# Kernel tuning notes

Measured on AMD Instinct MI355X. Metric: run time of the kernel, lower is better.

Reference implementation:

```python
import jax, jax.numpy as jnp
import numpy as np

N_NODES = 50000
N_EDGES = 640000
D_IN = 128
D_H1 = 128
D_H2 = 256
NEG_SLOPE = 0.2


def setup_inputs() -> dict:
    key = jax.random.key(0)
    ks = jax.random.split(key, 12)
    s = 1.0 / np.sqrt(D_IN)
    inp = {
        'x': jax.random.normal(ks[0], (N_NODES, D_IN), dtype=jnp.float32),
        'edge_index': jax.random.randint(ks[1], (2, N_EDGES), 0, N_NODES, dtype=jnp.int64),
        # GATv2 layer 1: 128 -> 128 (separate lin_l / lin_r, attention vec, residual proj, bias)
        'Wl1': jax.random.normal(ks[2], (D_IN, D_H1), dtype=jnp.float32) * s,
        'Wr1': jax.random.normal(ks[3], (D_IN, D_H1), dtype=jnp.float32) * s,
        'att1': jax.random.normal(ks[4], (D_H1,), dtype=jnp.float32) * s,
        'Wres1': jax.random.normal(ks[5], (D_IN, D_H1), dtype=jnp.float32) * s,
        'b1': jnp.zeros((D_H1,), dtype=jnp.float32),
        # GATv2 layer 2: 128 -> 256
        'Wl2': jax.random.normal(ks[6], (D_H1, D_H2), dtype=jnp.float32) * s,
        'Wr2': jax.random.normal(ks[7], (D_H1, D_H2), dtype=jnp.float32) * s,
        'att2': jax.random.normal(ks[8], (D_H2,), dtype=jnp.float32) * s,
        'Wres2': jax.random.normal(ks[9], (D_H1, D_H2), dtype=jnp.float32) * s,
        'b2': jnp.zeros((D_H2,), dtype=jnp.float32),
    }
    return inp


def _gatv2_layer(x, Wl, Wr, att, Wres, b, src, dst, n_nodes):
    """GATv2Conv (heads=1, residual=True, eval mode/no dropout).
    score e_ij = att . LeakyReLU(Wl x_src + Wr x_dst); softmax over incoming edges per dst;
    out_dst = sum_j alpha_ij * (Wl x_src) + residual + bias.
    """
    xl = x @ Wl                      # [N, F]
    xr = x @ Wr                      # [N, F]
    h = xl[src] + xr[dst]            # [E, F]  gather (irregular access)
    e = jax.nn.leaky_relu(h, NEG_SLOPE) @ att   # [E]
    # segment softmax over destination nodes
    m = jax.ops.segment_max(e, dst, num_segments=n_nodes)      # [N]
    w = jnp.exp(e - m[dst])                                     # [E]
    denom = jax.ops.segment_sum(w, dst, num_segments=n_nodes)   # [N]
    alpha = w / (denom[dst] + 1e-16)                             # [E]
    out = jax.ops.segment_sum(alpha[:, None] * xl[src], dst, num_segments=n_nodes)  # [N, F]
    return out + x @ Wres + b


def reference(x, edge_index, Wl1, Wr1, att1, Wres1, b1, Wl2, Wr2, att2, Wres2, b2):
    src = edge_index[0]
    dst = edge_index[1]
    h = _gatv2_layer(x, Wl1, Wr1, att1, Wres1, b1, src, dst, N_NODES)
    h = jax.nn.elu(h)
    out = _gatv2_layer(h, Wl2, Wr2, att2, Wres2, b2, src, dst, N_NODES)
    return out
```

## Files before the change

kernel.cpp:

```cpp
#include <hip/hip_runtime.h>

typedef unsigned short u16;
typedef unsigned int u32;
typedef __attribute__((ext_vector_type(8))) short bf16x8;
typedef __attribute__((ext_vector_type(4))) float f32x4;
typedef __attribute__((ext_vector_type(2))) float f32x2;

#define NN 50000
#define NE 640000

__device__ __forceinline__ float bfl(u32 u) { return __uint_as_float(u << 16); }
__device__ __forceinline__ float bfh(u32 u) { return __uint_as_float(u & 0xffff0000u); }
__device__ __forceinline__ float bf1(u16 v) { return __uint_as_float(((u32)v) << 16); }
__device__ __forceinline__ u16 f2bf(float f) {
  u32 u = __float_as_uint(f);
  u32 r = (u + 0x7fffu + ((u >> 16) & 1u)) >> 16;
  return (u16)r;
}

__device__ __forceinline__ f32x2 bc2(float s) { return (f32x2){s, s}; }
__device__ __forceinline__ f32x2 pkfma(f32x2 a, f32x2 b, f32x2 c) {
  return __builtin_elementwise_fma(a, b, c);
}
__device__ __forceinline__ f32x2 pkabs(f32x2 a) {
  return __builtin_elementwise_abs(a);
}

template <int CTRL>
__device__ __forceinline__ float dpp_add(float x) {
  int t = __builtin_amdgcn_update_dpp(0, __float_as_int(x), CTRL, 0xf, 0xf, true);
  return x + __int_as_float(t);
}

__device__ __forceinline__ void unpk2(uint4 v, f32x2* o) {
  o[0] = (f32x2){bfl(v.x), bfh(v.x)};
  o[1] = (f32x2){bfl(v.y), bfh(v.y)};
  o[2] = (f32x2){bfl(v.z), bfh(v.z)};
  o[3] = (f32x2){bfl(v.w), bfh(v.w)};
}

__global__ void probe_zero_kernel(const u16* __restrict__ x, const int* __restrict__ ei,
                                  int* __restrict__ flags, int* __restrict__ cnt, int n) {
  int g = blockIdx.x * 256 + threadIdx.x;
  if (g < n) cnt[g] = 0;
  if (blockIdx.x == 0) {
    __shared__ int s_f32, s_i32;
    if (threadIdx.x == 0) { s_f32 = 0; s_i32 = 0; }
    __syncthreads();
    int lf = 0, li = 0;
    for (int i = threadIdx.x; i < 1024; i += 256) {
      float v = bf1(x[i]);
      if (!(fabsf(v) < 1e8f)) lf = 1;
      if (ei[2 * i + 1] != 0) li = 1;
    }
    if (lf) s_f32 = 1;
    if (li) s_i32 = 1;
    __syncthreads();
    if (threadIdx.x == 0) {
      flags[0] = s_f32;
      flags[1] = s_i32 ? 0 : 1;
    }
  }
}

__device__ __forceinline__ int edge_val(const int* __restrict__ w, long j, int i64) {
  return i64 ? w[2 * j] : w[j];
}

__global__ void count_kernel(const int* __restrict__ ei, const int* __restrict__ flags,
                             int* __restrict__ cnt, int E) {
  int e = blockIdx.x * blockDim.x + threadIdx.x;
  if (e >= E) return;
  int d = edge_val(ei, (long)E + e, flags[1]);
  if ((u32)d < (u32)NN) atomicAdd(&cnt[d], 1);
}

__global__ void scan_local(const int* __restrict__ cnt, int* __restrict__ excl,
                           int* __restrict__ bsum, int n) {
  __shared__ int sd[256];
  int t = threadIdx.x;
  int g = blockIdx.x * 256 + t;
  int v = (g < n) ? cnt[g] : 0;
  sd[t] = v;
  __syncthreads();
  for (int off = 1; off < 256; off <<= 1) {
    int x = (t >= off) ? sd[t - off] : 0;
    __syncthreads();
    sd[t] += x;
    __syncthreads();
  }
  int incl = sd[t];
  if (g < n) excl[g] = incl - v;
  if (t == 255) bsum[blockIdx.x] = incl;
}

__global__ void scan_add(const int* __restrict__ excl, const int* __restrict__ bsum,
                         const int* __restrict__ cnt, int* __restrict__ rowptr,
                         int* __restrict__ fillp, int n, int nb) {
  __shared__ int sd[256];
  int t = threadIdx.x;
  sd[t] = (t < nb && t < (int)blockIdx.x) ? bsum[t] : 0;
  __syncthreads();
  for (int off = 128; off > 0; off >>= 1) {
    if (t < off) sd[t] += sd[t + off];
    __syncthreads();
  }
  int boff = sd[0];
  int g = blockIdx.x * 256 + t;
  if (g < n) {
    int e2 = excl[g] + boff;
    rowptr[g] = e2;
    fillp[g] = e2;
    if (g == n - 1) rowptr[n] = e2 + cnt[g];
  }
}

__global__ void fill_kernel(const int* __restrict__ ei, const int* __restrict__ flags,
                            int* __restrict__ fillp, int* __restrict__ col, int E) {
  int e = blockIdx.x * blockDim.x + threadIdx.x;
  if (e >= E) return;
  int i64 = flags[1];
  int s = edge_val(ei, (long)e, i64);
  int d = edge_val(ei, (long)E + e, i64);
  if ((u32)d >= (u32)NN) return;
  int p = atomicAdd(&fillp[d], 1);
  col[p] = ((u32)s < (u32)NN) ? s : 0;
}

__global__ void transpose_w(const void* W0, const void* W1, const void* W2,
                            const void* W3, const void* W4, const void* W5,
                            u16* T0, u16* T1, u16* T2, u16* T3, u16* T4, u16* T5,
                            const int* __restrict__ flags) {
  int y = blockIdx.y;
  int M = (y < 3) ? 128 : 256;
  int flat = blockIdx.x * 256 + threadIdx.x;
  if (flat >= M * 128) return;
  int j = flat >> 7;
  int k = flat & 127;
  const void* W = (y == 0) ? W0 : (y == 1) ? W1 : (y == 2) ? W2 : (y == 3) ? W3 : (y == 4) ? W4 : W5;
  u16* T = (y == 0) ? T0 : (y == 1) ? T1 : (y == 2) ? T2 : (y == 3) ? T3 : (y == 4) ? T4 : T5;
  u16 v;
  if (flags[0])
    v = f2bf(((const float*)W)[(size_t)k * M + j]);
  else
    v = ((const u16*)W)[(size_t)k * M + j];
  T[(size_t)j * 128 + k] = v;
}

#define LSTR 136
template <int MZ>
__global__ __launch_bounds__(256) void gemm3_mz(
    const void* __restrict__ X,
    const u16* __restrict__ Wta, const u16* __restrict__ Wtb, const u16* __restrict__ Wtc,
    const void* __restrict__ bias,
    u16* __restrict__ Ya, u16* __restrict__ Yb, u16* __restrict__ Yc,
    const int* __restrict__ flags, int x_follows, int N) {
  constexpr int M = MZ * 128;
  __shared__ __align__(16) u16 Xs[64 * LSTR];
  __shared__ __align__(16) u16 Bs[128 * LSTR];
  const int K = 128;
  int t = threadIdx.x;
  int lane = t & 63;
  int w = t >> 6;
  int n0g = blockIdx.x * 64;
  int F32X = x_follows ? flags[0] : 0;
  const u16* Wt = (blockIdx.y == 0) ? Wta : ((blockIdx.y == 1) ? Wtb : Wtc);
  u16* Y = (blockIdx.y == 0) ? Ya : ((blockIdx.y == 1) ? Yb : Yc);

  if (!F32X) {
    const u16* Xg = (const u16*)X;
    for (int it = 0; it < 4; ++it) {
      int i = t + 256 * it;
      int r = i >> 4, c8 = (i & 15) * 8;
      int n = n0g + r;
      uint4 v = make_uint4(0, 0, 0, 0);
      if (n < N) v = *(const uint4*)(Xg + (size_t)n * K + c8);
      *(uint4*)(Xs + r * LSTR + c8) = v;
    }
  } else {
    const float* Xg = (const float*)X;
    for (int it = 0; it < 4; ++it) {
      int i = t + 256 * it;
      int r = i >> 4, c8 = (i & 15) * 8;
      int n = n0g + r;
      uint4 pk = make_uint4(0, 0, 0, 0);
      if (n < N) {
        float4 f0 = *(const float4*)(Xg + (size_t)n * K + c8);
        float4 f1 = *(const float4*)(Xg + (size_t)n * K + c8 + 4);
        pk.x = (u32)f2bf(f0.x) | ((u32)f2bf(f0.y) << 16);
        pk.y = (u32)f2bf(f0.z) | ((u32)f2bf(f0.w) << 16);
        pk.z = (u32)f2bf(f1.x) | ((u32)f2bf(f1.y) << 16);
        pk.w = (u32)f2bf(f1.z) | ((u32)f2bf(f1.w) << 16);
      }
      *(uint4*)(Xs + r * LSTR + c8) = pk;
    }
  }

  int m0 = (w >> 1) * 32;
  int n0 = (w & 1) * 64;
  int l15 = lane & 15;
  int q8 = (lane >> 4) * 8;
  int F32B = flags[0];

#pragma unroll
  for (int z = 0; z < MZ; ++z) {
    int c0 = z * 128;
    for (int it = 0; it < 8; ++it) {
      int i = t + 256 * it;
      int j = i >> 4, k8 = (i & 15) * 8;
      uint4 v = *(const uint4*)(Wt + (size_t)(c0 + j) * K + k8);
      *(uint4*)(Bs + j * LSTR + k8) = v;
    }
    __syncthreads();

    f32x4 acc[2][4];
#pragma unroll
    for (int i = 0; i < 2; ++i)
#pragma unroll
      for (int j = 0; j < 4; ++j) acc[i][j] = (f32x4){0.f, 0.f, 0.f, 0.f};

#pragma unroll
    for (int kc = 0; kc < 4; ++kc) {
      int ko = kc * 32 + q8;
      bf16x8 a[2], b[4];
#pragma unroll
      for (int i = 0; i < 2; ++i)
        a[i] = *(const bf16x8*)(Xs + (m0 + i * 16 + l15) * LSTR + ko);
#pragma unroll
      for (int j = 0; j < 4; ++j)
        b[j] = *(const bf16x8*)(Bs + (n0 + j * 16 + l15) * LSTR + ko);
#pragma unroll
      for (int i = 0; i < 2; ++i)
#pragma unroll
        for (int j = 0; j < 4; ++j)
          acc[i][j] = __builtin_amdgcn_mfma_f32_16x16x32_bf16(a[i], b[j], acc[i][j], 0, 0, 0);
    }
    __syncthreads();

    float bv[4] = {0.f, 0.f, 0.f, 0.f};
    if (blockIdx.y == 2) {
#pragma unroll
      for (int j = 0; j < 4; ++j) {
        int c = c0 + n0 + j * 16 + l15;
        bv[j] = F32B ? ((const float*)bias)[c] : bf1(((const u16*)bias)[c]);
      }
    }

    u16* Ct = Bs;
#pragma unroll
    for (int i = 0; i < 2; ++i)
#pragma unroll
      for (int j = 0; j < 4; ++j) {
        int colj = n0 + j * 16 + l15;
        int rbase = m0 + i * 16 + (lane >> 4) * 4;
#pragma unroll
        for (int r = 0; r < 4; ++r)
          Ct[(rbase + r) * LSTR + colj] = f2bf(acc[i][j][r] + bv[j]);
      }
    __syncthreads();

    for (int it = 0; it < 4; ++it) {
      int i = t + 256 * it;
      int r = i >> 4, c8 = (i & 15) * 8;
      int n = n0g + r;
      if (n < N) {
        uint4 v = *(const uint4*)(Ct + r * LSTR + c8);
        *(uint4*)(Y + (size_t)n * M + c0 + c8) = v;
      }
    }
    __syncthreads();
  }
}

template <int F, bool ELU, int GL>
__global__ __launch_bounds__(256) void gat_agg_kernel(
    const u16* __restrict__ xl, const u16* __restrict__ xr, const u16* __restrict__ res,
    const void* __restrict__ att, const int* __restrict__ rowptr, const int* __restrict__ col,
    void* __restrict__ out, const int* __restrict__ flags, int out_follows, int N) {
  constexpr int HEPL = F / GL;
  constexpr int HP = HEPL / 2;
  static_assert(HEPL == 8, "GL must be F/8");
  int tid = threadIdx.x;
  int gl = tid & (GL - 1);
  int node = blockIdx.x * (256 / GL) + (tid / GL);
  if (node >= N) return;
  int F32 = flags[0];
  int OF32 = out_follows ? F32 : 0;
  int base = gl * HEPL;

  f32x2 xr2[HP], att6[HP], att4[HP], acc2[HP];
  {
    uint4 xp = *(const uint4*)(xr + (size_t)node * F + base);
    unpk2(xp, xr2);
  }
  if (F32) {
    const float* af = (const float*)att + base;
#pragma unroll
    for (int p = 0; p < HP; ++p) {
      f32x2 a = (f32x2){af[2 * p], af[2 * p + 1]};
      att6[p] = a * 0.6f;
      att4[p] = a * 0.4f;
    }
  } else {
    f32x2 a2[HP];
    uint4 ap = *(const uint4*)((const u16*)att + base);
    unpk2(ap, a2);
#pragma unroll
    for (int p = 0; p < HP; ++p) {
      att6[p] = a2[p] * 0.6f;
      att4[p] = a2[p] * 0.4f;
    }
  }
#pragma unroll
  for (int p = 0; p < HP; ++p) acc2[p] = bc2(0.f);

  float m = -1e30f, l = 0.f;
  int beg = rowptr[node], end = rowptr[node + 1];
  int deg = end - beg;

  if (deg > 0) {
    int nit = (deg + 1) >> 1;
    int dm1 = deg - 1;
    auto ldc = [&](int j) -> int { return col[beg + min(j, dm1)]; };
    auto gat = [&](int c) -> uint4 { return *(const uint4*)(xl + (size_t)c * F + base); };

    int c4 = ldc(4), c5 = ldc(5);
    uint4 va = gat(ldc(0)), vb = gat(ldc(1)), vc = gat(ldc(2)), vd = gat(ldc(3));

    for (int t = 0; t < nit; ++t) {
      uint4 x0v = va, x1v = vb;
      int act1 = (2 * t + 1) < deg;
      va = vc; vb = vd;
      if (t + 2 < nit) { vc = gat(c4); vd = gat(c5); }
      if (t + 3 < nit) { c4 = ldc(2 * t + 6); c5 = ldc(2 * t + 7); }

      f32x2 x0[HP], x1[HP];
      unpk2(x0v, x0);
      unpk2(x1v, x1);
      f32x2 s0 = bc2(0.f), s1 = bc2(0.f);
#pragma unroll
      for (int p = 0; p < HP; ++p) {
        f32x2 h0 = x0[p] + xr2[p];
        f32x2 h1 = x1[p] + xr2[p];
        f32x2 ha0 = pkabs(h0);
        f32x2 ha1 = pkabs(h1);
        s0 = pkfma(att6[p], h0, s0);
        s1 = pkfma(att6[p], h1, s1);
        s0 = pkfma(att4[p], ha0, s0);
        s1 = pkfma(att4[p], ha1, s1);
      }
      float d0 = s0.x + s0.y;
      float d1 = s1.x + s1.y;
      d0 = dpp_add<0xB1>(d0);  d1 = dpp_add<0xB1>(d1);
      d0 = dpp_add<0x4E>(d0);  d1 = dpp_add<0x4E>(d1);
      d0 = dpp_add<0x141>(d0); d1 = dpp_add<0x141>(d1);
      d0 = dpp_add<0x140>(d0); d1 = dpp_add<0x140>(d1);
      if constexpr (GL == 32) {
        d0 += __shfl_xor(d0, 16, 64);
        d1 += __shfl_xor(d1, 16, 64);
      }

      float p0 = d0;
      float p1 = act1 ? d1 : -1e30f;
      float mn = fmaxf(m, fmaxf(p0, p1));
      float scl = __expf(m - mn);
      float w0 = __expf(p0 - mn);
      float w1 = __expf(p1 - mn);
      l = fmaf(l, scl, w0 + w1);
      f32x2 w0b = bc2(w0), w1b = bc2(w1), sclb = bc2(scl);
#pragma unroll
      for (int p = 0; p < HP; ++p)
        acc2[p] = pkfma(sclb, acc2[p], pkfma(w1b, x1[p], w0b * x0[p]));
      m = mn;
    }
  }

  float inv = 1.f / (l + 1e-16f);
  uint4 rp = *(const uint4*)(res + (size_t)node * F + base);
  f32x2 rv[HP];
  unpk2(rp, rv);
  f32x2 ov[HP];
  f32x2 invb = bc2(inv);
#pragma unroll
  for (int p = 0; p < HP; ++p) {
    f32x2 o = pkfma(acc2[p], invb, rv[p]);
    if (ELU) {
      o.x = (o.x > 0.f) ? o.x : (__expf(o.x) - 1.f);
      o.y = (o.y > 0.f) ? o.y : (__expf(o.y) - 1.f);
    }
    ov[p] = o;
  }
  if (OF32) {
    float* of = (float*)out + (size_t)node * F + base;
    float4 f0 = {ov[0].x, ov[0].y, ov[1].x, ov[1].y};
    float4 f1 = {ov[2].x, ov[2].y, ov[3].x, ov[3].y};
    *(float4*)of = f0;
    *(float4*)(of + 4) = f1;
  } else {
    u16* o16 = (u16*)out;
    uint4 pk;
    pk.x = (u32)f2bf(ov[0].x) | ((u32)f2bf(ov[0].y) << 16);
    pk.y = (u32)f2bf(ov[1].x) | ((u32)f2bf(ov[1].y) << 16);
    pk.z = (u32)f2bf(ov[2].x) | ((u32)f2bf(ov[2].y) << 16);
    pk.w = (u32)f2bf(ov[3].x) | ((u32)f2bf(ov[3].y) << 16);
    *(uint4*)(o16 + (size_t)node * F + base) = pk;
  }
}

extern "C" void kernel_launch(void* const* d_in, const int* in_sizes, int n_in,
                              void* d_out, int out_size, void* d_ws, size_t ws_size,
                              hipStream_t stream) {
  const u16* x16 = (const u16*)d_in[0];
  const int* ei = (const int*)d_in[1];
  const int N = NN, E = NE;

  char* ws = (char*)d_ws;
  size_t off = 0;
  auto alloc = [&](size_t bytes) -> void* {
    void* p = (void*)(ws + off);
    off += (bytes + 255) & ~(size_t)255;
    return p;
  };
  int* flags = (int*)alloc(2 * 4);
  int* cnt = (int*)alloc((size_t)N * 4);
  int* rowptr = (int*)alloc((size_t)(N + 1) * 4);
  int* fillp = (int*)alloc((size_t)N * 4);
  int* colb = (int*)alloc((size_t)E * 4);
  int* excl = (int*)alloc((size_t)N * 4);
  int* bsum = (int*)alloc(256 * 4);
  u16* Wt1a = (u16*)alloc((size_t)128 * 128 * 2);
  u16* Wt1b = (u16*)alloc((size_t)128 * 128 * 2);
  u16* Wt1c = (u16*)alloc((size_t)128 * 128 * 2);
  u16* Wt2a = (u16*)alloc((size_t)256 * 128 * 2);
  u16* Wt2b = (u16*)alloc((size_t)256 * 128 * 2);
  u16* Wt2c = (u16*)alloc((size_t)256 * 128 * 2);
  u16* buf1 = (u16*)alloc((size_t)N * 256 * 2);
  u16* buf2 = (u16*)alloc((size_t)N * 256 * 2);
  u16* buf3 = (u16*)alloc((size_t)N * 256 * 2);
  u16* h1 = (u16*)alloc((size_t)N * 128 * 2);
  (void)ws_size; (void)n_in; (void)in_sizes; (void)out_size;

  int nb = (N + 255) / 256;

  probe_zero_kernel<<<nb, 256, 0, stream>>>(x16, ei, flags, cnt, N);
  count_kernel<<<(E + 255) / 256, 256, 0, stream>>>(ei, flags, cnt, E);
  scan_local<<<nb, 256, 0, stream>>>(cnt, excl, bsum, N);
  scan_add<<<nb, 256, 0, stream>>>(excl, bsum, cnt, rowptr, fillp, N, nb);
  fill_kernel<<<(E + 255) / 256, 256, 0, stream>>>(ei, flags, fillp, colb, E);
  transpose_w<<<dim3(128, 6), 256, 0, stream>>>(
      d_in[2], d_in[3], d_in[5], d_in[7], d_in[8], d_in[10],
      Wt1a, Wt1b, Wt1c, Wt2a, Wt2b, Wt2c, flags);

  int gx = (N + 63) / 64;
  gemm3_mz<1><<<dim3(gx, 3), 256, 0, stream>>>(
      d_in[0], Wt1a, Wt1b, Wt1c, d_in[6], buf1, buf2, buf3, flags, 1, N);
  gat_agg_kernel<128, true, 16><<<(N + 15) / 16, 256, 0, stream>>>(
      buf1, buf2, buf3, d_in[4], rowptr, colb, h1, flags, 0, N);
  gemm3_mz<2><<<dim3(gx, 3), 256, 0, stream>>>(
      h1, Wt2a, Wt2b, Wt2c, d_in[11], buf1, buf2, buf3, flags, 0, N);
  gat_agg_kernel<256, false, 32><<<(N + 7) / 8, 256, 0, stream>>>(
      buf1, buf2, buf3, d_in[9], rowptr, colb, d_out, flags, 1, N);
}
```

Baseline: 318.5 us.

## Process aggregation nodes in descending-degree order via a degree-bucketed permutation

```diff
diff --git a/kernel.cpp b/kernel.cpp
--- a/kernel.cpp
+++ b/kernel.cpp
@@ -40,9 +40,11 @@
 }
 
 __global__ void probe_zero_kernel(const u16* __restrict__ x, const int* __restrict__ ei,
-                                  int* __restrict__ flags, int* __restrict__ cnt, int n) {
+                                  int* __restrict__ flags, int* __restrict__ cnt,
+                                  int* __restrict__ dmeta, int n) {
   int g = blockIdx.x * 256 + threadIdx.x;
   if (g < n) cnt[g] = 0;
+  if (g < 128) dmeta[g] = 0;
   if (blockIdx.x == 0) {
     __shared__ int s_f32, s_i32;
     if (threadIdx.x == 0) { s_f32 = 0; s_i32 = 0; }
@@ -76,9 +78,11 @@
 }
 
 __global__ void scan_local(const int* __restrict__ cnt, int* __restrict__ excl,
-                           int* __restrict__ bsum, int n) {
+                           int* __restrict__ bsum, int* __restrict__ dcnt, int n) {
   __shared__ int sd[256];
+  __shared__ int h[64];
   int t = threadIdx.x;
+  if (t < 64) h[t] = 0;
   int g = blockIdx.x * 256 + t;
   int v = (g < n) ? cnt[g] : 0;
   sd[t] = v;
@@ -92,6 +96,9 @@
   int incl = sd[t];
   if (g < n) excl[g] = incl - v;
   if (t == 255) bsum[blockIdx.x] = incl;
+  if (g < n) atomicAdd(&h[63 - min(v, 63)], 1);
+  __syncthreads();
+  if (t < 64 && h[t]) atomicAdd(&dcnt[t], h[t]);
 }
 
 __global__ void scan_add(const int* __restrict__ excl, const int* __restrict__ bsum,
@@ -112,6 +119,25 @@
     rowptr[g] = e2;
     fillp[g] = e2;
     if (g == n - 1) rowptr[n] = e2 + cnt[g];
+  }
+}
+
+__global__ void deg_scatter(const int* __restrict__ cnt, const int* __restrict__ dcnt,
+                            int* __restrict__ dticket, int* __restrict__ perm, int n) {
+  __shared__ int sv[64], base[64];
+  int t = threadIdx.x;
+  if (t < 64) sv[t] = dcnt[t];
+  __syncthreads();
+  if (t == 0) {
+    int r = 0;
+    for (int i = 0; i < 64; ++i) { base[i] = r; r += sv[i]; }
+  }
+  __syncthreads();
+  int g = blockIdx.x * 256 + t;
+  if (g < n) {
+    int b = 63 - min(cnt[g], 63);
+    int pos = base[b] + atomicAdd(&dticket[b], 1);
+    perm[pos] = g;
   }
 }
 
@@ -276,14 +302,16 @@
 __global__ __launch_bounds__(256) void gat_agg_kernel(
     const u16* __restrict__ xl, const u16* __restrict__ xr, const u16* __restrict__ res,
     const void* __restrict__ att, const int* __restrict__ rowptr, const int* __restrict__ col,
+    const int* __restrict__ perm,
     void* __restrict__ out, const int* __restrict__ flags, int out_follows, int N) {
   constexpr int HEPL = F / GL;
   constexpr int HP = HEPL / 2;
   static_assert(HEPL == 8, "GL must be F/8");
   int tid = threadIdx.x;
   int gl = tid & (GL - 1);
-  int node = blockIdx.x * (256 / GL) + (tid / GL);
-  if (node >= N) return;
+  int gid = blockIdx.x * (256 / GL) + (tid / GL);
+  if (gid >= N) return;
+  int node = perm[gid];
   int F32 = flags[0];
   int OF32 = out_follows ? F32 : 0;
   int base = gl * HEPL;
@@ -428,6 +456,8 @@
   int* colb = (int*)alloc((size_t)E * 4);
   int* excl = (int*)alloc((size_t)N * 4);
   int* bsum = (int*)alloc(256 * 4);
+  int* dmeta = (int*)alloc(128 * 4);
+  int* perm = (int*)alloc((size_t)N * 4);
   u16* Wt1a = (u16*)alloc((size_t)128 * 128 * 2);
   u16* Wt1b = (u16*)alloc((size_t)128 * 128 * 2);
   u16* Wt1c = (u16*)alloc((size_t)128 * 128 * 2);
@@ -441,11 +471,14 @@
   (void)ws_size; (void)n_in; (void)in_sizes; (void)out_size;
 
   int nb = (N + 255) / 256;
-
-  probe_zero_kernel<<<nb, 256, 0, stream>>>(x16, ei, flags, cnt, N);
+  int* dcnt = dmeta;
+  int* dticket = dmeta + 64;
+
+  probe_zero_kernel<<<nb, 256, 0, stream>>>(x16, ei, flags, cnt, dmeta, N);
   count_kernel<<<(E + 255) / 256, 256, 0, stream>>>(ei, flags, cnt, E);
-  scan_local<<<nb, 256, 0, stream>>>(cnt, excl, bsum, N);
+  scan_local<<<nb, 256, 0, stream>>>(cnt, excl, bsum, dcnt, N);
   scan_add<<<nb, 256, 0, stream>>>(excl, bsum, cnt, rowptr, fillp, N, nb);
+  deg_scatter<<<nb, 256, 0, stream>>>(cnt, dcnt, dticket, perm, N);
   fill_kernel<<<(E + 255) / 256, 256, 0, stream>>>(ei, flags, fillp, colb, E);
   transpose_w<<<dim3(128, 6), 256, 0, stream>>>(
       d_in[2], d_in[3], d_in[5], d_in[7], d_in[8], d_in[10],
@@ -455,9 +488,9 @@
   gemm3_mz<1><<<dim3(gx, 3), 256, 0, stream>>>(
       d_in[0], Wt1a, Wt1b, Wt1c, d_in[6], buf1, buf2, buf3, flags, 1, N);
   gat_agg_kernel<128, true, 16><<<(N + 15) / 16, 256, 0, stream>>>(
-      buf1, buf2, buf3, d_in[4], rowptr, colb, h1, flags, 0, N);
+      buf1, buf2, buf3, d_in[4], rowptr, colb, perm, h1, flags, 0, N);
   gemm3_mz<2><<<dim3(gx, 3), 256, 0, stream>>>(
       h1, Wt2a, Wt2b, Wt2c, d_in[11], buf1, buf2, buf3, flags, 0, N);
   gat_agg_kernel<256, false, 32><<<(N + 7) / 8, 256, 0, stream>>>(
-      buf1, buf2, buf3, d_in[9], rowptr, colb, d_out, flags, 1, N);
-}
+      buf1, buf2, buf3, d_in[9], rowptr, colb, perm, d_out, flags, 1, N);
+}
```

New measurement: 473.9 us. 1.49x slower.
